# Kernel tuning notes

Hardware: AMD Instinct MI355X
Metric: run time of the kernel (lower is better)

Reference implementation:

```python
import jax, jax.numpy as jnp
import numpy as np

NUM_HEADS = 16  # from init_kwargs


def setup_inputs() -> dict:
    key = jax.random.key(0)
    k1, k2, k3, k4, k5 = jax.random.split(key, 5)
    B, N, C = 2, 2048, 1024
    return {
        "query": jax.random.normal(k1, (B, N, C), dtype=jnp.float32),
        "key": jax.random.normal(k2, (B, N, C), dtype=jnp.float32),
        "value": jax.random.normal(k3, (B, N, C), dtype=jnp.float32),
        "W_merge": jax.random.normal(k4, (C, C), dtype=jnp.float32) * (1.0 / np.sqrt(C)),
        "b_merge": jax.random.normal(k5, (C,), dtype=jnp.float32) * 0.02,
    }


def reference(query, key, value, W_merge, b_merge):
    B, N, C = query.shape
    H = NUM_HEADS
    dim = C // H
    # Faithful to torch: plain reshape (B,N,C) -> (B, dim, H, N), no transpose.
    q = query.reshape(B, dim, H, -1)
    k = key.reshape(B, dim, H, -1)
    v = value.reshape(B, dim, H, -1)
    # Faithful scale: divide by sqrt(N) (sequence length), as in the source.
    scale = 1.0 / np.sqrt(N).astype(np.float32)
    scores = jnp.einsum('bdhn,bdhm->bhnm', q, k) * scale  # [B,H,N,N]
    attn = jax.nn.softmax(scores, axis=-1)
    x = jnp.einsum('bhnm,bdhm->bdhn', attn, v)  # [B,dim,H,N]
    x = x.reshape(B, C, -1)  # [B,C,N]
    # Conv1d(C,C,kernel_size=1) == pointwise channel matmul + bias
    out = jnp.einsum('oc,bcn->bon', W_merge, x) + b_merge[None, :, None]
    return out  # [B,C,N]
```

## Files before the change

kernel.cpp:

```cpp
#include <hip/hip_runtime.h>


#define H 16
#define DIM 64
#define NSEQ 2048
#define CCH 1024
#define BATCH 2
#define DSTR (H * NSEQ)
#define PSP 72

typedef __attribute__((ext_vector_type(8))) short bf16x8;
typedef __attribute__((ext_vector_type(4))) float f32x4;

__device__ __forceinline__ unsigned short f2bf(float x) {
  unsigned int u = __builtin_bit_cast(unsigned int, x);
  u += 0x7FFFu + ((u >> 16) & 1u);
  return (unsigned short)(u >> 16);
}

__device__ __forceinline__ unsigned int pack2bf(float a, float b) {
#if __has_builtin(__builtin_amdgcn_cvt_pk_bf16_f32)
  typedef __attribute__((ext_vector_type(2))) __bf16 bf16x2_t;
  bf16x2_t r = __builtin_amdgcn_cvt_pk_bf16_f32(a, b);
  return __builtin_bit_cast(unsigned int, r);
#else
  unsigned int ua = __builtin_bit_cast(unsigned int, a);
  unsigned int ub = __builtin_bit_cast(unsigned int, b);
  ua += 0x7FFFu + ((ua >> 16) & 1u);
  ub += 0x7FFFu + ((ub >> 16) & 1u);
  return __builtin_amdgcn_perm(ub, ua, 0x07060302u);
#endif
}

__device__ __forceinline__ float fast_exp2(float x) {
#if __has_builtin(__builtin_amdgcn_exp2f)
  return __builtin_amdgcn_exp2f(x);
#else
  return exp2f(x);
#endif
}

__device__ __forceinline__ void gld16(const void* g, void* l) {
  __builtin_amdgcn_global_load_lds(
      (const __attribute__((address_space(1))) unsigned int*)g,
      (__attribute__((address_space(3))) unsigned int*)l, 16, 0, 0);
}

__global__ __launch_bounds__(256) void prep_w(const float* __restrict__ W,
                                              unsigned short* __restrict__ Wp) {
  int idx = blockIdx.x * 256 + threadIdx.x;
  int o = idx >> 10, cp = idx & 1023;
  int hh = cp >> 6, d = cp & 63;
  Wp[idx] = f2bf(W[o * CCH + d * H + hh]);
}

__global__ __launch_bounds__(256) void conv_v(const float* __restrict__ v,
                                              unsigned short* __restrict__ Vb) {
  int idx = blockIdx.x * 256 + threadIdx.x;
  float4 x = ((const float4*)v)[idx];
  ushort4 o;
  o.x = f2bf(x.x); o.y = f2bf(x.y); o.z = f2bf(x.z); o.w = f2bf(x.w);
  ((ushort4*)Vb)[idx] = o;
}

__global__ __launch_bounds__(256) void prep_tr(const float* __restrict__ q,
                                               const float* __restrict__ k,
                                               unsigned short* __restrict__ Qt,
                                               unsigned short* __restrict__ Kt) {
  __shared__ unsigned short T[64][72];
  const int tid = threadIdx.x;
  const int n0 = blockIdx.x * 64;
  const int hh = blockIdx.y;
  const int b = blockIdx.z >> 1, t = blockIdx.z & 1;
  const float* src = t ? k : q;
  unsigned short* dst = t ? Kt : Qt;
  const float scl = t ? 1.0f : (0.022097086912079608f * 1.4426950408889634f);
  const size_t base = (size_t)b * (CCH * NSEQ) + (size_t)hh * NSEQ;
#pragma unroll
  for (int it = 0; it < 4; ++it) {
    int i4 = it * 256 + tid;
    int d = i4 >> 4;
    int nn = (i4 & 15) << 2;
    float4 val = *(const float4*)(src + base + (size_t)d * DSTR + n0 + nn);
    T[nn + 0][d] = f2bf(val.x * scl);
    T[nn + 1][d] = f2bf(val.y * scl);
    T[nn + 2][d] = f2bf(val.z * scl);
    T[nn + 3][d] = f2bf(val.w * scl);
  }
  __syncthreads();
  const size_t obase = ((size_t)(b * H + hh) * NSEQ + n0) * 64;
#pragma unroll
  for (int it = 0; it < 2; ++it) {
    int idx = it * 256 + tid;
    int row = idx >> 3, cb = idx & 7;
    *(bf16x8*)(dst + obase + (size_t)row * 64 + cb * 8) = *(const bf16x8*)&T[row][cb * 8];
  }
}

__global__ __launch_bounds__(256) void attn3(const unsigned short* __restrict__ Qt,
                                             const unsigned short* __restrict__ Kt,
                                             const unsigned short* __restrict__ Vb,
                                             unsigned short* __restrict__ xt) {
  __shared__ __align__(16) unsigned short Ks[2][64 * 64];
  __shared__ __align__(16) unsigned short Vs[2][64 * 64];
  __shared__ __align__(16) unsigned short UQ[4 * 32 * PSP];
  unsigned short* Qs = UQ;
  unsigned short* Ps = UQ;

  const int tid = threadIdx.x;
  const int w = tid >> 6, lane = tid & 63;
  const int quad = lane >> 4, l16 = lane & 15;
  const int n0 = blockIdx.x * 128;
  const int hh = blockIdx.y, b = blockIdx.z;

  const unsigned short* Qbase = Qt + ((size_t)(b * H + hh) * NSEQ + n0) * 64;
  const unsigned short* Kbase = Kt + ((size_t)(b * H + hh) * NSEQ) * 64;
  const unsigned short* Vbase = Vb + (size_t)b * (CCH * NSEQ) + (size_t)hh * NSEQ;

  const int srow = w * 8 + (lane >> 3);
  const int scb = lane & 7;

#pragma unroll
  for (int i = 0; i < 4; ++i) {
    int row = i * 32 + srow;
    int cbl = scb ^ (row & 7);
    gld16(Qbase + (size_t)row * 64 + cbl * 8, &Qs[(i * 32 + w * 8) * 64]);
  }
#pragma unroll
  for (int i = 0; i < 2; ++i) {
    int row = i * 32 + srow;
    int cbl = scb ^ (row & 7);
    gld16(Kbase + (size_t)row * 64 + cbl * 8, &Ks[0][(i * 32 + w * 8) * 64]);
    gld16(Vbase + (size_t)row * DSTR + cbl * 8, &Vs[0][(i * 32 + w * 8) * 64]);
  }
  __syncthreads();

  bf16x8 bQ[2][2];
#pragma unroll
  for (int nt = 0; nt < 2; ++nt)
#pragma unroll
    for (int kh = 0; kh < 2; ++kh) {
      int row = w * 32 + nt * 16 + l16;
      int phys = (kh * 4 + quad) ^ (l16 & 7);
      bQ[nt][kh] = *(const bf16x8*)&Qs[(size_t)row * 64 + phys * 8];
    }
  __syncthreads();

  f32x4 O[2][4];
  float lsum[2] = {0.f, 0.f};
#pragma unroll
  for (int nt = 0; nt < 2; ++nt)
#pragma unroll
    for (int dt = 0; dt < 4; ++dt) O[nt][dt] = (f32x4){0.f, 0.f, 0.f, 0.f};

  const int psw = w * 32 * PSP;

  for (int it = 0; it < 32; ++it) {
    const int cur = it & 1;
    if (it + 1 < 32) {
      const int nxt = cur ^ 1;
      const int m0n = (it + 1) * 64;
#pragma unroll
      for (int i = 0; i < 2; ++i) {
        int row = i * 32 + srow;
        int cbl = scb ^ (row & 7);
        gld16(Kbase + (size_t)(m0n + row) * 64 + cbl * 8, &Ks[nxt][(i * 32 + w * 8) * 64]);
        gld16(Vbase + (size_t)row * DSTR + m0n + cbl * 8, &Vs[nxt][(i * 32 + w * 8) * 64]);
      }
    }

    f32x4 St[4][2];
#pragma unroll
    for (int mt = 0; mt < 4; ++mt)
#pragma unroll
      for (int nt = 0; nt < 2; ++nt) St[mt][nt] = (f32x4){0.f, 0.f, 0.f, 0.f};
#pragma unroll
    for (int mt = 0; mt < 4; ++mt)
#pragma unroll
      for (int kh = 0; kh < 2; ++kh) {
        int row = mt * 16 + l16;
        int phys = (kh * 4 + quad) ^ (l16 & 7);
        bf16x8 aK = *(const bf16x8*)&Ks[cur][(size_t)row * 64 + phys * 8];
        St[mt][0] = __builtin_amdgcn_mfma_f32_16x16x32_bf16(aK, bQ[0][kh], St[mt][0], 0, 0, 0);
        St[mt][1] = __builtin_amdgcn_mfma_f32_16x16x32_bf16(aK, bQ[1][kh], St[mt][1], 0, 0, 0);
      }

#pragma unroll
    for (int nt = 0; nt < 2; ++nt) {
#pragma unroll
      for (int mt = 0; mt < 4; ++mt) {
        float e0 = fast_exp2(St[mt][nt][0]);
        float e1 = fast_exp2(St[mt][nt][1]);
        float e2 = fast_exp2(St[mt][nt][2]);
        float e3 = fast_exp2(St[mt][nt][3]);
        lsum[nt] += (e0 + e1) + (e2 + e3);
        uint2 pk;
        pk.x = pack2bf(e0, e1);
        pk.y = pack2bf(e2, e3);
        *(uint2*)&Ps[psw + (nt * 16 + l16) * PSP + mt * 16 + quad * 4] = pk;
      }
    }

    bf16x8 aP[2][2];
#pragma unroll
    for (int nt = 0; nt < 2; ++nt)
#pragma unroll
      for (int kh = 0; kh < 2; ++kh)
        aP[nt][kh] = *(const bf16x8*)&Ps[psw + (nt * 16 + l16) * PSP + kh * 32 + quad * 8];
#pragma unroll
    for (int dt = 0; dt < 4; ++dt)
#pragma unroll
      for (int kh = 0; kh < 2; ++kh) {
        int row = dt * 16 + l16;
        int phys = (kh * 4 + quad) ^ (l16 & 7);
        bf16x8 bV = *(const bf16x8*)&Vs[cur][(size_t)row * 64 + phys * 8];
        O[0][dt] = __builtin_amdgcn_mfma_f32_16x16x32_bf16(aP[0][kh], bV, O[0][dt], 0, 0, 0);
        O[1][dt] = __builtin_amdgcn_mfma_f32_16x16x32_bf16(aP[1][kh], bV, O[1][dt], 0, 0, 0);
      }

    __syncthreads();
  }

#pragma unroll
  for (int nt = 0; nt < 2; ++nt) {
    lsum[nt] += __shfl_xor(lsum[nt], 16, 64);
    lsum[nt] += __shfl_xor(lsum[nt], 32, 64);
  }

  const size_t xb = (size_t)b * ((size_t)NSEQ * CCH);
#pragma unroll
  for (int nt = 0; nt < 2; ++nt)
#pragma unroll
    for (int r = 0; r < 4; ++r) {
      float inv = 1.0f / __shfl(lsum[nt], quad * 4 + r, 64);
      int n = n0 + w * 32 + nt * 16 + quad * 4 + r;
#pragma unroll
      for (int dt = 0; dt < 4; ++dt) {
        int cp = hh * 64 + dt * 16 + l16;
        xt[xb + (size_t)n * CCH + cp] = f2bf(O[nt][dt][r] * inv);
      }
    }
}

__global__ __launch_bounds__(256) void merge2(const unsigned short* __restrict__ Wp,
                                              const unsigned short* __restrict__ xt,
                                              const float* __restrict__ bias,
                                              float* __restrict__ out) {
  __shared__ unsigned short At[128 * 64];
  __shared__ unsigned short Bt[128 * 64];
  const int tid = threadIdx.x;
  const int w = tid >> 6, lane = tid & 63;
  const int quad = lane >> 4, l16 = lane & 15;
  const int wx = w & 1, wy = w >> 1;
  const int n0 = blockIdx.x * 128, o0 = blockIdx.y * 128, b = blockIdx.z;
  const int srow = w * 8 + (lane >> 3), scb = lane & 7;
  const unsigned short* Bbase = xt + (size_t)b * ((size_t)NSEQ * CCH);

  f32x4 acc[4][4];
#pragma unroll
  for (int ot = 0; ot < 4; ++ot)
#pragma unroll
    for (int nt = 0; nt < 4; ++nt) acc[ot][nt] = (f32x4){0.f, 0.f, 0.f, 0.f};

  for (int c0 = 0; c0 < CCH; c0 += 64) {
    __syncthreads();
#pragma unroll
    for (int i = 0; i < 4; ++i) {
      int row = i * 32 + srow;
      int cbl = scb ^ (row & 7);
      gld16(Wp + (size_t)(o0 + row) * CCH + c0 + cbl * 8, &At[(i * 32 + w * 8) * 64]);
      gld16(Bbase + (size_t)(n0 + row) * CCH + c0 + cbl * 8, &Bt[(i * 32 + w * 8) * 64]);
    }
    __syncthreads();
#pragma unroll
    for (int ks = 0; ks < 2; ++ks) {
      bf16x8 aW[4], bX[4];
      int phys = ((ks * 4 + quad) ^ (l16 & 7)) * 8;
#pragma unroll
      for (int t = 0; t < 4; ++t) {
        aW[t] = *(const bf16x8*)&At[(wy * 64 + t * 16 + l16) * 64 + phys];
        bX[t] = *(const bf16x8*)&Bt[(wx * 64 + t * 16 + l16) * 64 + phys];
      }
#pragma unroll
      for (int ot = 0; ot < 4; ++ot)
#pragma unroll
        for (int nt = 0; nt < 4; ++nt)
          acc[ot][nt] = __builtin_amdgcn_mfma_f32_16x16x32_bf16(aW[ot], bX[nt], acc[ot][nt], 0, 0, 0);
    }
  }

#pragma unroll
  for (int ot = 0; ot < 4; ++ot)
#pragma unroll
    for (int r = 0; r < 4; ++r) {
      int o = o0 + wy * 64 + ot * 16 + quad * 4 + r;
      float bi = bias[o];
#pragma unroll
      for (int nt = 0; nt < 4; ++nt)
        out[(size_t)b * ((size_t)CCH * NSEQ) + (size_t)o * NSEQ + n0 + wx * 64 + nt * 16 + l16] =
            acc[ot][nt][r] + bi;
    }
}

extern "C" void kernel_launch(void* const* d_in, const int* in_sizes, int n_in,
                              void* d_out, int out_size, void* d_ws, size_t ws_size,
                              hipStream_t stream) {
  const float* q = (const float*)d_in[0];
  const float* k = (const float*)d_in[1];
  const float* v = (const float*)d_in[2];
  const float* W = (const float*)d_in[3];
  const float* bias = (const float*)d_in[4];
  float* out = (float*)d_out;

  unsigned short* Wp = (unsigned short*)d_ws;
  unsigned short* xt = Wp + (1u << 20);
  unsigned short* Qt = xt + (4u << 20);
  unsigned short* Kt = Qt + (4u << 20);
  unsigned short* Vb = Kt + (4u << 20);

  hipLaunchKernelGGL(prep_w, dim3(4096), dim3(256), 0, stream, W, Wp);
  hipLaunchKernelGGL(conv_v, dim3(4096), dim3(256), 0, stream, v, Vb);
  hipLaunchKernelGGL(prep_tr, dim3(NSEQ / 64, H, BATCH * 2), dim3(256), 0, stream,
                     q, k, Qt, Kt);
  hipLaunchKernelGGL(attn3, dim3(NSEQ / 128, H, BATCH), dim3(256), 0, stream,
                     Qt, Kt, Vb, xt);
  hipLaunchKernelGGL(merge2, dim3(NSEQ / 128, CCH / 128, BATCH), dim3(256), 0, stream,
                     Wp, xt, bias, out);
}
```

Before: 191.6 us.

## Rewrite attention with 32x32 MFMA, split-KV warp groups, and double-buffer merge GEMM

The attention kernel moves from 16x16x32 to 32x32x16 bf16 MFMA. It keeps the exponentiated scores in registers, rearranged with permlane32 swaps, instead of going through an LDS P buffer. Each 512-thread block covers 256 queries and splits the KV sequence between two warp groups, then combines partial outputs and row sums through LDS. The merge GEMM gains a double-buffered LDS prefetch of the next K chunk. The trade-off is higher register and LDS pressure and a cross-group reduction step, while the grid shrinks to 256 attention blocks.

Result: faster. 177.9 us (-7.1%).

```diff
diff --git a/kernel.cpp b/kernel.cpp
--- a/kernel.cpp
+++ b/kernel.cpp
@@ -7,10 +7,11 @@
 #define CCH 1024
 #define BATCH 2
 #define DSTR (H * NSEQ)
-#define PSP 72
 
 typedef __attribute__((ext_vector_type(8))) short bf16x8;
 typedef __attribute__((ext_vector_type(4))) float f32x4;
+typedef __attribute__((ext_vector_type(16))) float f32x16;
+typedef __attribute__((ext_vector_type(4))) unsigned int uint32x4;
 
 __device__ __forceinline__ unsigned short f2bf(float x) {
   unsigned int u = __builtin_bit_cast(unsigned int, x);
@@ -40,10 +41,34 @@
 #endif
 }
 
+__device__ __forceinline__ void permswap32(unsigned int& a, unsigned int& b) {
+#if __has_builtin(__builtin_amdgcn_permlane32_swap)
+  typedef __attribute__((ext_vector_type(2))) unsigned int uint2v;
+  uint2v r = __builtin_amdgcn_permlane32_swap(a, b, false, false);
+  a = r[0];
+  b = r[1];
+#else
+  unsigned int ax = (unsigned int)__shfl_xor((int)a, 32, 64);
+  unsigned int bx = (unsigned int)__shfl_xor((int)b, 32, 64);
+  bool lo = (threadIdx.x & 63) < 32;
+  unsigned int na = lo ? a : bx;
+  unsigned int nb = lo ? ax : b;
+  a = na;
+  b = nb;
+#endif
+}
+
 __device__ __forceinline__ void gld16(const void* g, void* l) {
   __builtin_amdgcn_global_load_lds(
       (const __attribute__((address_space(1))) unsigned int*)g,
       (__attribute__((address_space(3))) unsigned int*)l, 16, 0, 0);
+}
+
+__device__ __forceinline__ f32x16 zero16() {
+  f32x16 v;
+#pragma unroll
+  for (int i = 0; i < 16; ++i) v[i] = 0.f;
+  return v;
 }
 
 __global__ __launch_bounds__(256) void prep_w(const float* __restrict__ W,
@@ -97,157 +122,195 @@
   }
 }
 
-__global__ __launch_bounds__(256) void attn3(const unsigned short* __restrict__ Qt,
-                                             const unsigned short* __restrict__ Kt,
-                                             const unsigned short* __restrict__ Vb,
-                                             unsigned short* __restrict__ xt) {
-  __shared__ __align__(16) unsigned short Ks[2][64 * 64];
-  __shared__ __align__(16) unsigned short Vs[2][64 * 64];
-  __shared__ __align__(16) unsigned short UQ[4 * 32 * PSP];
-  unsigned short* Qs = UQ;
-  unsigned short* Ps = UQ;
+__global__ __launch_bounds__(512, 2) void attn4(const unsigned short* __restrict__ Qt,
+                                                const unsigned short* __restrict__ Kt,
+                                                const unsigned short* __restrict__ Vb,
+                                                unsigned short* __restrict__ xt) {
+  __shared__ __align__(16) unsigned char sbuf[65536 + 2048];
+  unsigned short* KV = (unsigned short*)sbuf;
+  float* lsumLDS = (float*)(sbuf + 65536);
+  float* Oex = (float*)sbuf;
 
   const int tid = threadIdx.x;
   const int w = tid >> 6, lane = tid & 63;
-  const int quad = lane >> 4, l16 = lane & 15;
-  const int n0 = blockIdx.x * 128;
+  const int lane31 = lane & 31, hl = lane >> 5;
+  const int g = w >> 2, nw = w & 3;
+  const int n0 = blockIdx.x * 256;
   const int hh = blockIdx.y, b = blockIdx.z;
 
   const unsigned short* Qbase = Qt + ((size_t)(b * H + hh) * NSEQ + n0) * 64;
-  const unsigned short* Kbase = Kt + ((size_t)(b * H + hh) * NSEQ) * 64;
-  const unsigned short* Vbase = Vb + (size_t)b * (CCH * NSEQ) + (size_t)hh * NSEQ;
-
-  const int srow = w * 8 + (lane >> 3);
-  const int scb = lane & 7;
+  const unsigned short* Kg = Kt + ((size_t)(b * H + hh) * NSEQ + g * 1024) * 64;
+  const unsigned short* Vg = Vb + (size_t)b * (CCH * NSEQ) + (size_t)hh * NSEQ + g * 1024;
+
+  const int r8 = lane >> 3, scb = lane & 7;
 
 #pragma unroll
   for (int i = 0; i < 4; ++i) {
-    int row = i * 32 + srow;
+    int row = i * 64 + w * 8 + r8;
     int cbl = scb ^ (row & 7);
-    gld16(Qbase + (size_t)row * 64 + cbl * 8, &Qs[(i * 32 + w * 8) * 64]);
-  }
+    gld16(Qbase + (size_t)row * 64 + cbl * 8, KV + (i * 64 + w * 8) * 64);
+  }
+  __syncthreads();
+
+  bf16x8 bQ[2][4];
+#pragma unroll
+  for (int nt = 0; nt < 2; ++nt)
+#pragma unroll
+    for (int ks = 0; ks < 4; ++ks) {
+      int row = nw * 64 + nt * 32 + lane31;
+      int phys = (ks * 2 + hl) ^ (row & 7);
+      bQ[nt][ks] = *(const bf16x8*)(KV + (size_t)row * 64 + phys * 8);
+    }
+  __syncthreads();
+
+#define KVOFF(gg, bb, kk) ((((gg)*2 + (bb)) * 2 + (kk)) * 4096)
+
 #pragma unroll
   for (int i = 0; i < 2; ++i) {
-    int row = i * 32 + srow;
+    int row = i * 32 + nw * 8 + r8;
     int cbl = scb ^ (row & 7);
-    gld16(Kbase + (size_t)row * 64 + cbl * 8, &Ks[0][(i * 32 + w * 8) * 64]);
-    gld16(Vbase + (size_t)row * DSTR + cbl * 8, &Vs[0][(i * 32 + w * 8) * 64]);
-  }
-  __syncthreads();
-
-  bf16x8 bQ[2][2];
+    gld16(Kg + (size_t)row * 64 + cbl * 8, KV + KVOFF(g, 0, 0) + (i * 32 + nw * 8) * 64);
+    gld16(Vg + (size_t)row * DSTR + cbl * 8, KV + KVOFF(g, 0, 1) + (i * 32 + nw * 8) * 64);
+  }
+  __syncthreads();
+
+  f32x16 O[2][2];
 #pragma unroll
   for (int nt = 0; nt < 2; ++nt)
 #pragma unroll
-    for (int kh = 0; kh < 2; ++kh) {
-      int row = w * 32 + nt * 16 + l16;
-      int phys = (kh * 4 + quad) ^ (l16 & 7);
-      bQ[nt][kh] = *(const bf16x8*)&Qs[(size_t)row * 64 + phys * 8];
-    }
-  __syncthreads();
-
-  f32x4 O[2][4];
+    for (int dt = 0; dt < 2; ++dt) O[nt][dt] = zero16();
   float lsum[2] = {0.f, 0.f};
-#pragma unroll
-  for (int nt = 0; nt < 2; ++nt)
-#pragma unroll
-    for (int dt = 0; dt < 4; ++dt) O[nt][dt] = (f32x4){0.f, 0.f, 0.f, 0.f};
-
-  const int psw = w * 32 * PSP;
-
-  for (int it = 0; it < 32; ++it) {
+
+  for (int it = 0; it < 16; ++it) {
     const int cur = it & 1;
-    if (it + 1 < 32) {
+    if (it < 15) {
       const int nxt = cur ^ 1;
       const int m0n = (it + 1) * 64;
 #pragma unroll
       for (int i = 0; i < 2; ++i) {
-        int row = i * 32 + srow;
+        int row = i * 32 + nw * 8 + r8;
         int cbl = scb ^ (row & 7);
-        gld16(Kbase + (size_t)(m0n + row) * 64 + cbl * 8, &Ks[nxt][(i * 32 + w * 8) * 64]);
-        gld16(Vbase + (size_t)row * DSTR + m0n + cbl * 8, &Vs[nxt][(i * 32 + w * 8) * 64]);
-      }
-    }
-
-    f32x4 St[4][2];
-#pragma unroll
-    for (int mt = 0; mt < 4; ++mt)
-#pragma unroll
-      for (int nt = 0; nt < 2; ++nt) St[mt][nt] = (f32x4){0.f, 0.f, 0.f, 0.f};
-#pragma unroll
-    for (int mt = 0; mt < 4; ++mt)
-#pragma unroll
-      for (int kh = 0; kh < 2; ++kh) {
-        int row = mt * 16 + l16;
-        int phys = (kh * 4 + quad) ^ (l16 & 7);
-        bf16x8 aK = *(const bf16x8*)&Ks[cur][(size_t)row * 64 + phys * 8];
-        St[mt][0] = __builtin_amdgcn_mfma_f32_16x16x32_bf16(aK, bQ[0][kh], St[mt][0], 0, 0, 0);
-        St[mt][1] = __builtin_amdgcn_mfma_f32_16x16x32_bf16(aK, bQ[1][kh], St[mt][1], 0, 0, 0);
-      }
-
-#pragma unroll
-    for (int nt = 0; nt < 2; ++nt) {
-#pragma unroll
-      for (int mt = 0; mt < 4; ++mt) {
-        float e0 = fast_exp2(St[mt][nt][0]);
-        float e1 = fast_exp2(St[mt][nt][1]);
-        float e2 = fast_exp2(St[mt][nt][2]);
-        float e3 = fast_exp2(St[mt][nt][3]);
-        lsum[nt] += (e0 + e1) + (e2 + e3);
-        uint2 pk;
-        pk.x = pack2bf(e0, e1);
-        pk.y = pack2bf(e2, e3);
-        *(uint2*)&Ps[psw + (nt * 16 + l16) * PSP + mt * 16 + quad * 4] = pk;
-      }
-    }
-
-    bf16x8 aP[2][2];
+        gld16(Kg + (size_t)(m0n + row) * 64 + cbl * 8,
+              KV + KVOFF(g, nxt, 0) + (i * 32 + nw * 8) * 64);
+        gld16(Vg + (size_t)row * DSTR + m0n + cbl * 8,
+              KV + KVOFF(g, nxt, 1) + (i * 32 + nw * 8) * 64);
+      }
+    }
+
+#pragma unroll
+    for (int mt = 0; mt < 2; ++mt) {
+      f32x16 St[2];
+      St[0] = zero16();
+      St[1] = zero16();
+#pragma unroll
+      for (int ks = 0; ks < 4; ++ks) {
+        int row = mt * 32 + lane31;
+        int phys = (ks * 2 + hl) ^ (row & 7);
+        bf16x8 aK = *(const bf16x8*)(KV + KVOFF(g, cur, 0) + row * 64 + phys * 8);
+        St[0] = __builtin_amdgcn_mfma_f32_32x32x16_bf16(aK, bQ[0][ks], St[0], 0, 0, 0);
+        St[1] = __builtin_amdgcn_mfma_f32_32x32x16_bf16(aK, bQ[1][ks], St[1], 0, 0, 0);
+      }
+
+      unsigned int pd[2][8];
+#pragma unroll
+      for (int nt = 0; nt < 2; ++nt)
+#pragma unroll
+        for (int t = 0; t < 8; ++t) {
+          float e0 = fast_exp2(St[nt][2 * t]);
+          float e1 = fast_exp2(St[nt][2 * t + 1]);
+          lsum[nt] += e0 + e1;
+          pd[nt][t] = pack2bf(e0, e1);
+        }
+
+      unsigned int s[2][2][4];
+#pragma unroll
+      for (int nt = 0; nt < 2; ++nt) {
+        s[nt][0][0] = pd[nt][0]; s[nt][0][2] = pd[nt][2];
+        s[nt][0][1] = pd[nt][1]; s[nt][0][3] = pd[nt][3];
+        s[nt][1][0] = pd[nt][4]; s[nt][1][2] = pd[nt][6];
+        s[nt][1][1] = pd[nt][5]; s[nt][1][3] = pd[nt][7];
+        permswap32(s[nt][0][0], s[nt][0][2]);
+        permswap32(s[nt][0][1], s[nt][0][3]);
+        permswap32(s[nt][1][0], s[nt][1][2]);
+        permswap32(s[nt][1][1], s[nt][1][3]);
+      }
+
+#pragma unroll
+      for (int ms = 0; ms < 2; ++ms) {
+        bf16x8 bV[2];
+#pragma unroll
+        for (int dt = 0; dt < 2; ++dt) {
+          int row = dt * 32 + lane31;
+          int phys = (mt * 4 + ms * 2 + hl) ^ (row & 7);
+          bV[dt] = *(const bf16x8*)(KV + KVOFF(g, cur, 1) + row * 64 + phys * 8);
+        }
+#pragma unroll
+        for (int nt = 0; nt < 2; ++nt) {
+          bf16x8 aP = __builtin_bit_cast(
+              bf16x8, (uint32x4){s[nt][ms][0], s[nt][ms][1], s[nt][ms][2], s[nt][ms][3]});
+          O[nt][0] = __builtin_amdgcn_mfma_f32_32x32x16_bf16(aP, bV[0], O[nt][0], 0, 0, 0);
+          O[nt][1] = __builtin_amdgcn_mfma_f32_32x32x16_bf16(aP, bV[1], O[nt][1], 0, 0, 0);
+        }
+      }
+    }
+    __syncthreads();
+  }
+
+#pragma unroll
+  for (int nt = 0; nt < 2; ++nt) lsum[nt] += __shfl_xor(lsum[nt], 32, 64);
+  if (hl == 0) {
 #pragma unroll
     for (int nt = 0; nt < 2; ++nt)
-#pragma unroll
-      for (int kh = 0; kh < 2; ++kh)
-        aP[nt][kh] = *(const bf16x8*)&Ps[psw + (nt * 16 + l16) * PSP + kh * 32 + quad * 8];
-#pragma unroll
-    for (int dt = 0; dt < 4; ++dt)
-#pragma unroll
-      for (int kh = 0; kh < 2; ++kh) {
-        int row = dt * 16 + l16;
-        int phys = (kh * 4 + quad) ^ (l16 & 7);
-        bf16x8 bV = *(const bf16x8*)&Vs[cur][(size_t)row * 64 + phys * 8];
-        O[0][dt] = __builtin_amdgcn_mfma_f32_16x16x32_bf16(aP[0][kh], bV, O[0][dt], 0, 0, 0);
-        O[1][dt] = __builtin_amdgcn_mfma_f32_16x16x32_bf16(aP[1][kh], bV, O[1][dt], 0, 0, 0);
-      }
-
-    __syncthreads();
-  }
-
-#pragma unroll
-  for (int nt = 0; nt < 2; ++nt) {
-    lsum[nt] += __shfl_xor(lsum[nt], 16, 64);
-    lsum[nt] += __shfl_xor(lsum[nt], 32, 64);
-  }
-
-  const size_t xb = (size_t)b * ((size_t)NSEQ * CCH);
-#pragma unroll
-  for (int nt = 0; nt < 2; ++nt)
-#pragma unroll
-    for (int r = 0; r < 4; ++r) {
-      float inv = 1.0f / __shfl(lsum[nt], quad * 4 + r, 64);
-      int n = n0 + w * 32 + nt * 16 + quad * 4 + r;
-#pragma unroll
-      for (int dt = 0; dt < 4; ++dt) {
-        int cp = hh * 64 + dt * 16 + l16;
-        xt[xb + (size_t)n * CCH + cp] = f2bf(O[nt][dt][r] * inv);
-      }
-    }
-}
-
-__global__ __launch_bounds__(256) void merge2(const unsigned short* __restrict__ Wp,
-                                              const unsigned short* __restrict__ xt,
-                                              const float* __restrict__ bias,
-                                              float* __restrict__ out) {
-  __shared__ unsigned short At[128 * 64];
-  __shared__ unsigned short Bt[128 * 64];
+      lsumLDS[g * 256 + nw * 64 + nt * 32 + lane31] = lsum[nt];
+  }
+  if (g == 1) {
+#pragma unroll
+    for (int nt = 0; nt < 2; ++nt)
+#pragma unroll
+      for (int dt = 0; dt < 2; ++dt)
+#pragma unroll
+        for (int r = 0; r < 16; ++r) {
+          int nl = nw * 64 + nt * 32 + (r & 3) + 8 * (r >> 2) + 4 * hl;
+          Oex[nl * 64 + dt * 32 + lane31] = O[nt][dt][r];
+        }
+  }
+  __syncthreads();
+  if (g == 0) {
+    const size_t xb = (size_t)b * ((size_t)NSEQ * CCH);
+#pragma unroll
+    for (int nt = 0; nt < 2; ++nt)
+#pragma unroll
+      for (int rq = 0; rq < 4; ++rq) {
+        int nlb = nw * 64 + nt * 32 + rq * 8 + 4 * hl;
+        float4 l0 = *(const float4*)&lsumLDS[nlb];
+        float4 l1 = *(const float4*)&lsumLDS[256 + nlb];
+        float inv0 = 1.0f / (l0.x + l1.x);
+        float inv1 = 1.0f / (l0.y + l1.y);
+        float inv2 = 1.0f / (l0.z + l1.z);
+        float inv3 = 1.0f / (l0.w + l1.w);
+#pragma unroll
+        for (int dt = 0; dt < 2; ++dt) {
+          int d = dt * 32 + lane31;
+#pragma unroll
+          for (int rr = 0; rr < 4; ++rr) {
+            int r = rq * 4 + rr;
+            float val = O[nt][dt][r] + Oex[(nlb + rr) * 64 + d];
+            float inv = (rr == 0) ? inv0 : (rr == 1) ? inv1 : (rr == 2) ? inv2 : inv3;
+            int n = n0 + nlb + rr;
+            xt[xb + (size_t)n * CCH + hh * 64 + d] = f2bf(val * inv);
+          }
+        }
+      }
+  }
+#undef KVOFF
+}
+
+__global__ __launch_bounds__(256, 2) void merge3(const unsigned short* __restrict__ Wp,
+                                                 const unsigned short* __restrict__ xt,
+                                                 const float* __restrict__ bias,
+                                                 float* __restrict__ out) {
+  __shared__ unsigned short At[2][128 * 64];
+  __shared__ unsigned short Bt[2][128 * 64];
   const int tid = threadIdx.x;
   const int w = tid >> 6, lane = tid & 63;
   const int quad = lane >> 4, l16 = lane & 15;
@@ -262,31 +325,45 @@
 #pragma unroll
     for (int nt = 0; nt < 4; ++nt) acc[ot][nt] = (f32x4){0.f, 0.f, 0.f, 0.f};
 
-  for (int c0 = 0; c0 < CCH; c0 += 64) {
-    __syncthreads();
-#pragma unroll
-    for (int i = 0; i < 4; ++i) {
-      int row = i * 32 + srow;
-      int cbl = scb ^ (row & 7);
-      gld16(Wp + (size_t)(o0 + row) * CCH + c0 + cbl * 8, &At[(i * 32 + w * 8) * 64]);
-      gld16(Bbase + (size_t)(n0 + row) * CCH + c0 + cbl * 8, &Bt[(i * 32 + w * 8) * 64]);
-    }
-    __syncthreads();
+#pragma unroll
+  for (int i = 0; i < 4; ++i) {
+    int row = i * 32 + srow;
+    int cbl = scb ^ (row & 7);
+    gld16(Wp + (size_t)(o0 + row) * CCH + cbl * 8, &At[0][(i * 32 + w * 8) * 64]);
+    gld16(Bbase + (size_t)(n0 + row) * CCH + cbl * 8, &Bt[0][(i * 32 + w * 8) * 64]);
+  }
+  __syncthreads();
+
+  for (int it = 0; it < 16; ++it) {
+    const int cur = it & 1;
+    if (it < 15) {
+      const int nxt = cur ^ 1;
+      const int c0 = (it + 1) * 64;
+#pragma unroll
+      for (int i = 0; i < 4; ++i) {
+        int row = i * 32 + srow;
+        int cbl = scb ^ (row & 7);
+        gld16(Wp + (size_t)(o0 + row) * CCH + c0 + cbl * 8, &At[nxt][(i * 32 + w * 8) * 64]);
+        gld16(Bbase + (size_t)(n0 + row) * CCH + c0 + cbl * 8, &Bt[nxt][(i * 32 + w * 8) * 64]);
+      }
+    }
 #pragma unroll
     for (int ks = 0; ks < 2; ++ks) {
       bf16x8 aW[4], bX[4];
       int phys = ((ks * 4 + quad) ^ (l16 & 7)) * 8;
 #pragma unroll
       for (int t = 0; t < 4; ++t) {
-        aW[t] = *(const bf16x8*)&At[(wy * 64 + t * 16 + l16) * 64 + phys];
-        bX[t] = *(const bf16x8*)&Bt[(wx * 64 + t * 16 + l16) * 64 + phys];
+        aW[t] = *(const bf16x8*)&At[cur][(wy * 64 + t * 16 + l16) * 64 + phys];
+        bX[t] = *(const bf16x8*)&Bt[cur][(wx * 64 + t * 16 + l16) * 64 + phys];
       }
 #pragma unroll
       for (int ot = 0; ot < 4; ++ot)
 #pragma unroll
         for (int nt = 0; nt < 4; ++nt)
-          acc[ot][nt] = __builtin_amdgcn_mfma_f32_16x16x32_bf16(aW[ot], bX[nt], acc[ot][nt], 0, 0, 0);
-    }
+          acc[ot][nt] =
+              __builtin_amdgcn_mfma_f32_16x16x32_bf16(aW[ot], bX[nt], acc[ot][nt], 0, 0, 0);
+    }
+    __syncthreads();
   }
 
 #pragma unroll
@@ -322,8 +399,8 @@
   hipLaunchKernelGGL(conv_v, dim3(4096), dim3(256), 0, stream, v, Vb);
   hipLaunchKernelGGL(prep_tr, dim3(NSEQ / 64, H, BATCH * 2), dim3(256), 0, stream,
                      q, k, Qt, Kt);
-  hipLaunchKernelGGL(attn3, dim3(NSEQ / 128, H, BATCH), dim3(256), 0, stream,
+  hipLaunchKernelGGL(attn4, dim3(NSEQ / 256, H, BATCH), dim3(512), 0, stream,
                      Qt, Kt, Vb, xt);
-  hipLaunchKernelGGL(merge2, dim3(NSEQ / 128, CCH / 128, BATCH), dim3(256), 0, stream,
+  hipLaunchKernelGGL(merge3, dim3(NSEQ / 128, CCH / 128, BATCH), dim3(256), 0, stream,
                      Wp, xt, bias, out);
 }
```
